# Kernel tuning notes

Measured on AMD Instinct MI355X. Metric: run time of the kernel, lower is better.

The kernel has to match this reference:

```python
import jax, jax.numpy as jnp
import numpy as np

WORD_DICT_SIZE = 50002
POS_DICT_SIZE = 53
DEP_DICT_SIZE = 54
EMB = 128
UNITS = 100
B, T = 256, 256
IN_DIM = 3 * EMB  # 384


def setup_inputs() -> dict:
    key = jax.random.key(0)
    ks = jax.random.split(key, 12)
    words = jax.random.randint(ks[0], (B, T), 1, WORD_DICT_SIZE)
    pos = jax.random.randint(ks[1], (B, T), 1, POS_DICT_SIZE)
    dep = jax.random.randint(ks[2], (B, T), 1, DEP_DICT_SIZE)
    # ragged padding: index 0 is the mask token (mask_zero=True)
    lengths = jax.random.randint(ks[3], (B,), T // 2, T + 1)
    pad = jnp.arange(T)[None, :] >= lengths[:, None]
    words = jnp.where(pad, 0, words)
    pos = jnp.where(pad, 0, pos)
    dep = jnp.where(pad, 0, dep)

    def glorot(k, shape):
        lim = np.sqrt(6.0 / (shape[0] + shape[1]))
        return jax.random.uniform(k, shape, jnp.float32, -lim, lim)

    E_word = glorot(ks[4], (WORD_DICT_SIZE, EMB))
    E_pos = glorot(ks[5], (POS_DICT_SIZE, EMB))
    E_dep = glorot(ks[6], (DEP_DICT_SIZE, EMB))
    W_fwd = glorot(ks[7], (IN_DIM, 4 * UNITS))
    U_fwd = glorot(ks[8], (UNITS, 4 * UNITS))
    W_bwd = glorot(ks[9], (IN_DIM, 4 * UNITS))
    U_bwd = glorot(ks[10], (UNITS, 4 * UNITS))
    # Keras unit_forget_bias=True: forget-gate bias initialized to 1
    b = jnp.zeros((4 * UNITS,), jnp.float32).at[UNITS:2 * UNITS].set(1.0)
    W_out = glorot(ks[11], (2 * UNITS, 1))
    b_out = jnp.zeros((1,), jnp.float32)
    return {"words": words, "pos": pos, "dep": dep,
            "E_word": E_word, "E_pos": E_pos, "E_dep": E_dep,
            "W_fwd": W_fwd, "U_fwd": U_fwd, "b_fwd": b,
            "W_bwd": W_bwd, "U_bwd": U_bwd, "b_bwd": b,
            "W_out": W_out, "b_out": b_out}


def _masked_lstm(x_tbd, mask_tb, W, U, b, reverse):
    """Keras-style masked LSTM. x_tbd: [T,B,D], mask_tb: [T,B].
    Masked steps carry state/output through unchanged (zero_output_for_mask=False)."""
    units = U.shape[0]
    xw = jnp.einsum('tbd,dh->tbh', x_tbd, W) + b  # precompute input projection

    def step(carry, inp):
        h, c = carry
        xw_t, m = inp
        z = xw_t + h @ U
        i, f, g, o = jnp.split(z, 4, axis=-1)
        i = jax.nn.sigmoid(i)
        f = jax.nn.sigmoid(f)
        g = jnp.tanh(g)
        o = jax.nn.sigmoid(o)
        c_new = f * c + i * g
        h_new = o * jnp.tanh(c_new)
        m = m[:, None]
        h2 = jnp.where(m, h_new, h)
        c2 = jnp.where(m, c_new, c)
        return (h2, c2), h2

    h0 = jnp.zeros((x_tbd.shape[1], units), x_tbd.dtype)
    _, hs = jax.lax.scan(step, (h0, h0), (xw, mask_tb), reverse=reverse)
    return hs  # [T,B,units]


def reference(words, pos, dep, E_word, E_pos, E_dep,
              W_fwd, U_fwd, b_fwd, W_bwd, U_bwd, b_bwd, W_out, b_out):
    mask = words != 0  # [B,T]
    x = jnp.concatenate([E_word[words], E_pos[pos], E_dep[dep]], axis=-1)  # [B,T,384]
    xt = jnp.transpose(x, (1, 0, 2))  # [T,B,384]
    mt = mask.T                        # [T,B]
    h_f = _masked_lstm(xt, mt, W_fwd, U_fwd, b_fwd, reverse=False)
    h_b = _masked_lstm(xt, mt, W_bwd, U_bwd, b_bwd, reverse=True)
    h = jnp.concatenate([h_f, h_b], axis=-1)          # [T,B,200]
    h = jnp.transpose(h, (1, 0, 2))                    # [B,T,200]
    out = jax.nn.sigmoid(h @ W_out + b_out)[..., 0]    # [B,T]
    return out
```

## Files before the change

### kernel.cpp

```cpp
#include <hip/hip_runtime.h>
#include <hip/hip_bf16.h>

#define T_LEN 256
#define B_SZ  256
#define EMB   128
#define UNITS 100
#define GATES 400
#define NCOL  800
#define NQ    52

typedef __attribute__((ext_vector_type(8))) short short8v;
typedef __attribute__((ext_vector_type(4))) short short4v;
typedef __attribute__((ext_vector_type(4))) float f32x4;
typedef _Float16 half2v __attribute__((ext_vector_type(2)));

static __device__ __forceinline__ float bf2f(short s) {
    unsigned u = ((unsigned)(unsigned short)s) << 16;
    return __builtin_bit_cast(float, u);
}
static __device__ __forceinline__ short f2bf(float f) {
    return __builtin_bit_cast(short, __float2bfloat16(f));
}
static __device__ __forceinline__ float fast_sigmoid(float x) {
    return 1.f / (1.f + __expf(-x));
}
static __device__ __forceinline__ float fast_tanh(float x) {
    return 1.f - 2.f / (1.f + __expf(2.f * x));
}
static __device__ __forceinline__ float fdot2p(unsigned hp, unsigned up, float c) {
#if __has_builtin(__builtin_amdgcn_fdot2)
    return __builtin_amdgcn_fdot2(__builtin_bit_cast(half2v, hp),
                                  __builtin_bit_cast(half2v, up), c, false);
#else
    const half2v a = __builtin_bit_cast(half2v, hp);
    const half2v b = __builtin_bit_cast(half2v, up);
    return fmaf((float)a[1], (float)b[1], fmaf((float)a[0], (float)b[0], c));
#endif
}

#define PREP_WT_BLOCKS 100
#define PREP_TAB_BLOCKS 107
#define PREP_UPK_BLOCKS 21

__global__ __launch_bounds__(256) void prep(
    const float* __restrict__ Wf, const float* __restrict__ Wb,
    const float* __restrict__ bf_, const float* __restrict__ bb_,
    const float* __restrict__ Ep, const float* __restrict__ Ed,
    const float* __restrict__ Uf, const float* __restrict__ Ub,
    __hip_bfloat16* __restrict__ WbT, float* __restrict__ Ppos,
    float* __restrict__ Pdep, unsigned* __restrict__ Upk, int* __restrict__ flag)
{
    __shared__ short Ap[16 * 32];
    __shared__ short Bp[32 * 16];

    const int bx = blockIdx.x, tid = threadIdx.x;

    if (bx < PREP_WT_BLOCKS) {
        const int base = bx * 1024 + tid * 4;
#pragma unroll
        for (int q = 0; q < 4; ++q) {
            const int id = base + q;
            const int c = id >> 7, k = id & 127;
            const int dir = c >= GATES;
            const int j = c - dir * GATES;
            const float* W = dir ? Wb : Wf;
            WbT[id] = __float2bfloat16(W[k * GATES + j]);
        }
    } else if (bx < PREP_WT_BLOCKS + PREP_TAB_BLOCKS) {
        const int p = bx - PREP_WT_BLOCKS;
        const bool isPos = p < 53;
        const float* Erow = isPos ? (Ep + p * EMB) : (Ed + (size_t)(p - 53) * EMB);
        const int rowoff = isPos ? EMB : 2 * EMB;
        float* dst = isPos ? (Ppos + (size_t)p * NCOL) : (Pdep + (size_t)(p - 53) * NCOL);
        for (int c = tid; c < NCOL; c += 256) {
            const int dir = c >= GATES;
            const int j = c - dir * GATES;
            const float* W = dir ? Wb : Wf;
            float s = 0.f;
            for (int k = 0; k < EMB; ++k)
                s = fmaf(Erow[k], W[(size_t)(rowoff + k) * GATES + j], s);
            if (!isPos) s += (dir ? bb_[j] : bf_[j]);
            dst[c] = s;
        }
    } else if (bx < PREP_WT_BLOCKS + PREP_TAB_BLOCKS + PREP_UPK_BLOCKS) {
        const int p2 = bx - PREP_WT_BLOCKS - PREP_TAB_BLOCKS;
#pragma unroll
        for (int i = 0; i < 8; ++i) {
            const int e = p2 * 2048 + tid * 8 + i;
            if (e < 2 * NQ * GATES) {
                const int dir = e / (NQ * GATES);
                const int rem = e - dir * (NQ * GATES);
                const int q = rem / GATES, col = rem - q * GATES;
                const float* U = dir ? Ub : Uf;
                const int k0 = 2 * q, k1 = 2 * q + 1;
                const float v0 = (k0 < UNITS) ? U[(size_t)k0 * GATES + col] : 0.f;
                const float v1 = (k1 < UNITS) ? U[(size_t)k1 * GATES + col] : 0.f;
                const unsigned lo = (unsigned)(unsigned short)__builtin_bit_cast(short, (_Float16)v0);
                const unsigned hi = (unsigned)(unsigned short)__builtin_bit_cast(short, (_Float16)v1);
                Upk[e] = lo | (hi << 16);
            }
        }
    } else {
        if (tid < 64) {
            for (int e = tid; e < 512; e += 64) {
                const int m = e >> 5, k = e & 31;
                Ap[e] = f2bf((float)((m * 3 + k * 5) % 7 - 3));
            }
            for (int e = tid; e < 512; e += 64) {
                const int k = e >> 4, n = e & 15;
                Bp[e] = f2bf((float)((k * 7 + n * 3) % 5 - 2));
            }
        }
        __syncthreads();
        if (tid < 64) {
            const int l = tid, mn = l & 15, grp = l >> 4;
            float ref[4];
#pragma unroll
            for (int i = 0; i < 4; ++i) {
                const int m = grp * 4 + i;
                float s = 0.f;
                for (int k = 0; k < 32; ++k)
                    s += bf2f(Ap[m * 32 + k]) * bf2f(Bp[k * 16 + mn]);
                ref[i] = s;
            }
            short8v a8, b8;
#pragma unroll
            for (int e = 0; e < 8; ++e) {
                const int k8 = grp * 8 + e;
                a8[e] = Ap[mn * 32 + k8];
                b8[e] = Bp[k8 * 16 + mn];
            }
            f32x4 z = {0.f, 0.f, 0.f, 0.f};
            f32x4 d8 = __builtin_amdgcn_mfma_f32_16x16x32_bf16(a8, b8, z, 0, 0, 0);
            const bool ok8 = (d8[0] == ref[0]) && (d8[1] == ref[1]) &&
                             (d8[2] == ref[2]) && (d8[3] == ref[3]);
            const unsigned long long m8 = __ballot(ok8);
            if (tid == 0) flag[0] = (m8 == ~0ULL) ? 0 : 1;
        }
    }
}

#define MT 64
#define NT 160

__global__ __launch_bounds__(256) void embed_gemm(
    const int* __restrict__ words, const int* __restrict__ pos, const int* __restrict__ dep,
    const float* __restrict__ Ew, const __hip_bfloat16* __restrict__ WbT,
    const float* __restrict__ Ppos, const float* __restrict__ Pdep,
    const int* __restrict__ flag, __hip_bfloat16* __restrict__ xw)
{
    __shared__ __align__(16) short As[MT * 128];
    __shared__ __align__(16) short Bs[NT * 128];
    __shared__ int widx[MT], pidx[MT], didx[MT];

    const int tid = threadIdx.x;
    const int bx = blockIdx.x, by = blockIdx.y;
    const int r0 = bx * MT;
    const int t = r0 >> 8, b0 = r0 & 255;
    const int n0 = by * NT;

    if (tid < MT)             widx[tid]          = words[(size_t)(b0 + tid) * T_LEN + t];
    else if (tid < 2 * MT)    pidx[tid - MT]     = pos[(size_t)(b0 + tid - MT) * T_LEN + t];
    else if (tid < 3 * MT)    didx[tid - 2 * MT] = dep[(size_t)(b0 + tid - 2 * MT) * T_LEN + t];
    __syncthreads();

#pragma unroll
    for (int q = 0; q < 4; ++q) {
        const int ch = tid + q * 256;
        const int row = ch >> 4, c16 = ch & 15;
        const float* src = Ew + (size_t)widx[row] * EMB + c16 * 8;
        const float4 v0 = *reinterpret_cast<const float4*>(src);
        const float4 v1 = *reinterpret_cast<const float4*>(src + 4);
        short8v pk;
        pk[0] = f2bf(v0.x); pk[1] = f2bf(v0.y); pk[2] = f2bf(v0.z); pk[3] = f2bf(v0.w);
        pk[4] = f2bf(v1.x); pk[5] = f2bf(v1.y); pk[6] = f2bf(v1.z); pk[7] = f2bf(v1.w);
        *reinterpret_cast<short8v*>(&As[row * 128 + ((c16 ^ (row & 7)) << 3)]) = pk;
    }
#pragma unroll
    for (int q = 0; q < 10; ++q) {
        const int ch = tid + q * 256;
        const int col = ch >> 4, c16 = ch & 15;
        const short* src = reinterpret_cast<const short*>(WbT) + (size_t)(n0 + col) * 128 + c16 * 8;
        const short8v v = *reinterpret_cast<const short8v*>(src);
        *reinterpret_cast<short8v*>(&Bs[col * 128 + ((c16 ^ (col & 7)) << 3)]) = v;
    }
    __syncthreads();

    const int w = tid >> 6, l = tid & 63;
    const int lr = l & 15, lg = l >> 4;
    const int arow = w * 16 + lr;

    f32x4 acc[10];
#pragma unroll
    for (int ni = 0; ni < 10; ++ni) acc[ni] = f32x4{0.f, 0.f, 0.f, 0.f};

    const int lay = flag[0];

    if (lay == 0) {
#pragma unroll
        for (int kk = 0; kk < 4; ++kk) {
            const int c16 = kk * 4 + lg;
            const short8v a = *reinterpret_cast<const short8v*>(
                &As[arow * 128 + ((c16 ^ (arow & 7)) << 3)]);
#pragma unroll
            for (int ni = 0; ni < 10; ++ni) {
                const int col = ni * 16 + lr;
                const short8v bfr = *reinterpret_cast<const short8v*>(
                    &Bs[col * 128 + ((c16 ^ (col & 7)) << 3)]);
                acc[ni] = __builtin_amdgcn_mfma_f32_16x16x32_bf16(a, bfr, acc[ni], 0, 0, 0);
            }
        }
    } else {
#pragma unroll
        for (int kk = 0; kk < 4; ++kk) {
            const int ch16 = kk * 4 + (lg >> 1);
            const int inner = (lg & 1) * 4;
            const int alo_i = arow * 128 + ((ch16 ^ (arow & 7)) << 3) + inner;
            const int ahi_i = arow * 128 + (((ch16 + 2) ^ (arow & 7)) << 3) + inner;
            const short4v alo = *reinterpret_cast<const short4v*>(&As[alo_i]);
            const short4v ahi = *reinterpret_cast<const short4v*>(&As[ahi_i]);
            short8v a;
            a[0] = alo[0]; a[1] = alo[1]; a[2] = alo[2]; a[3] = alo[3];
            a[4] = ahi[0]; a[5] = ahi[1]; a[6] = ahi[2]; a[7] = ahi[3];
#pragma unroll
            for (int ni = 0; ni < 10; ++ni) {
                const int col = ni * 16 + lr;
                const int blo_i = col * 128 + ((ch16 ^ (col & 7)) << 3) + inner;
                const int bhi_i = col * 128 + (((ch16 + 2) ^ (col & 7)) << 3) + inner;
                const short4v blo = *reinterpret_cast<const short4v*>(&Bs[blo_i]);
                const short4v bhi = *reinterpret_cast<const short4v*>(&Bs[bhi_i]);
                short8v b;
                b[0] = blo[0]; b[1] = blo[1]; b[2] = blo[2]; b[3] = blo[3];
                b[4] = bhi[0]; b[5] = bhi[1]; b[6] = bhi[2]; b[7] = bhi[3];
                acc[ni] = __builtin_amdgcn_mfma_f32_16x16x32_bf16(a, b, acc[ni], 0, 0, 0);
            }
        }
    }

    const int rbase = w * 16 + lg * 4;
    int pix[4], dix[4];
#pragma unroll
    for (int i = 0; i < 4; ++i) { pix[i] = pidx[rbase + i]; dix[i] = didx[rbase + i]; }
#pragma unroll
    for (int ni = 0; ni < 10; ++ni) {
        const int c = n0 + ni * 16 + lr;
#pragma unroll
        for (int i = 0; i < 4; ++i) {
            const float v = acc[ni][i]
                          + Ppos[(size_t)pix[i] * NCOL + c]
                          + Pdep[(size_t)dix[i] * NCOL + c];
            xw[(size_t)(r0 + rbase + i) * NCOL + c] = __float2bfloat16(v);
        }
    }
}

#define BAR() do { \
    asm volatile("s_waitcnt lgkmcnt(0)" ::: "memory"); \
    __builtin_amdgcn_sched_barrier(0); \
    __builtin_amdgcn_s_barrier(); \
    __builtin_amdgcn_sched_barrier(0); \
} while (0)

__global__ __launch_bounds__(512, 1) void lstm_valu(
    const int* __restrict__ words,
    const __hip_bfloat16* __restrict__ xw,
    const unsigned* __restrict__ Upk,
    _Float16* __restrict__ h_f, _Float16* __restrict__ h_b)
{
    const int b = blockIdx.x >> 1, dirv = blockIdx.x & 1;
    _Float16* hout = dirv ? h_b : h_f;
    const int coff = dirv * GATES;
    const unsigned* up = Upk + (size_t)dirv * NQ * GATES;

    __shared__ __align__(16) _Float16 h_sh[104];
    __shared__ float z_sh[GATES];
    __shared__ unsigned char m_sh[T_LEN];

    const int tid = threadIdx.x;
    const bool isCol = tid < GATES;
    const int colid = isCol ? tid : (GATES - 1);

    for (int i = tid; i < T_LEN; i += 512)
        m_sh[i] = (unsigned char)(words[(size_t)b * T_LEN + i] != 0);
    if (tid < 52) reinterpret_cast<unsigned*>(h_sh)[tid] = 0u;

    unsigned upk[NQ];
#pragma unroll
    for (int q = 0; q < NQ; ++q) upk[q] = up[q * GATES + colid];
#pragma unroll
    for (int q = 0; q < NQ; ++q) asm volatile("" : "+v"(upk[q]));

    float c = 0.f, h = 0.f;
    __syncthreads();

    const int t0 = dirv ? (T_LEN - 1) : 0;
    const int dt = dirv ? -1 : 1;
    const short* xs = reinterpret_cast<const short*>(xw);

    short pf = 0;
    if (isCol) pf = xs[((size_t)t0 * B_SZ + b) * NCOL + coff + tid];

    for (int s = 0; s < T_LEN; ++s) {
        const int t = t0 + dt * s;
        int tn = t + dt; tn = tn < 0 ? 0 : (tn > T_LEN - 1 ? T_LEN - 1 : tn);

        short pfn = pf;
        if (isCol) {
            const float zx = bf2f(pf);
            pfn = xs[((size_t)tn * B_SZ + b) * NCOL + coff + tid];
            float a0 = 0.f, a1 = 0.f, a2 = 0.f, a3 = 0.f;
            const uint4* h4 = reinterpret_cast<const uint4*>(h_sh);
#pragma unroll
            for (int qq = 0; qq < 13; ++qq) {
                const uint4 hv = h4[qq];
                a0 = fdot2p(hv.x, upk[4 * qq + 0], a0);
                a1 = fdot2p(hv.y, upk[4 * qq + 1], a1);
                a2 = fdot2p(hv.z, upk[4 * qq + 2], a2);
                a3 = fdot2p(hv.w, upk[4 * qq + 3], a3);
            }
            z_sh[tid] = zx + (a0 + a1) + (a2 + a3);
        }
        pf = pfn;

        BAR();

        if (tid < UNITS) {
            const float zi = z_sh[tid];
            const float zf = z_sh[tid + UNITS];
            const float zg = z_sh[tid + 2 * UNITS];
            const float zo = z_sh[tid + 3 * UNITS];
            const float ig = fast_sigmoid(zi);
            const float fg = fast_sigmoid(zf);
            const float gg = fast_tanh(zg);
            const float og = fast_sigmoid(zo);
            const float cn = fg * c + ig * gg;
            const float hn = og * fast_tanh(cn);
            const bool  m  = m_sh[t] != 0;
            h = m ? hn : h;
            c = m ? cn : c;
            const _Float16 hh = (_Float16)h;
            h_sh[tid] = hh;
            hout[((size_t)t * B_SZ + b) * UNITS + tid] = hh;
        }

        BAR();
    }
}

__global__ __launch_bounds__(256) void out_proj(
    const _Float16* __restrict__ h_f, const _Float16* __restrict__ h_b,
    const float* __restrict__ Wo, const float* __restrict__ bo,
    float* __restrict__ out)
{
    const int tid = threadIdx.x;
    const int g = tid >> 2, sub = tid & 3;
    const int r = blockIdx.x * 64 + g;
    const int t = r >> 8, b = r & 255;

    const _Float16* hf = h_f + (size_t)r * UNITS;
    const _Float16* hb = h_b + (size_t)r * UNITS;

    float s = 0.f;
    const int k0 = sub * 25;
#pragma unroll
    for (int k = 0; k < 25; ++k) s = fmaf((float)hf[k0 + k], Wo[k0 + k], s);
#pragma unroll
    for (int k = 0; k < 25; ++k) s = fmaf((float)hb[k0 + k], Wo[UNITS + k0 + k], s);

    s += __shfl_xor(s, 1);
    s += __shfl_xor(s, 2);

    if (sub == 0)
        out[(size_t)b * T_LEN + t] = 1.f / (1.f + __expf(-(s + bo[0])));
}

extern "C" void kernel_launch(void* const* d_in, const int* in_sizes, int n_in,
                              void* d_out, int out_size, void* d_ws, size_t ws_size,
                              hipStream_t stream)
{
    const int*   words = (const int*)d_in[0];
    const int*   pos   = (const int*)d_in[1];
    const int*   dep   = (const int*)d_in[2];
    const float* Ew    = (const float*)d_in[3];
    const float* Ep    = (const float*)d_in[4];
    const float* Ed    = (const float*)d_in[5];
    const float* Wf    = (const float*)d_in[6];
    const float* Uf    = (const float*)d_in[7];
    const float* bf_   = (const float*)d_in[8];
    const float* Wb    = (const float*)d_in[9];
    const float* Ub    = (const float*)d_in[10];
    const float* bb_   = (const float*)d_in[11];
    const float* Wo    = (const float*)d_in[12];
    const float* bo    = (const float*)d_in[13];
    float* out = (float*)d_out;

    auto alignup = [](size_t x) { return (x + 255) & ~(size_t)255; };
    char* p = (char*)d_ws;
    __hip_bfloat16* xw = (__hip_bfloat16*)p;  p += alignup((size_t)T_LEN * B_SZ * NCOL * 2);
    _Float16* h_f = (_Float16*)p;             p += alignup((size_t)T_LEN * B_SZ * UNITS * 2);
    _Float16* h_b = (_Float16*)p;             p += alignup((size_t)T_LEN * B_SZ * UNITS * 2);
    __hip_bfloat16* WbT = (__hip_bfloat16*)p; p += alignup((size_t)NCOL * 128 * 2);
    float* Ppos = (float*)p;                  p += alignup((size_t)53 * NCOL * 4);
    float* Pdep = (float*)p;                  p += alignup((size_t)54 * NCOL * 4);
    unsigned* Upk = (unsigned*)p;             p += alignup((size_t)2 * NQ * GATES * 4);
    int* flag = (int*)p;

    prep<<<dim3(PREP_WT_BLOCKS + PREP_TAB_BLOCKS + PREP_UPK_BLOCKS + 1), 256, 0, stream>>>(
        Wf, Wb, bf_, bb_, Ep, Ed, Uf, Ub, WbT, Ppos, Pdep, Upk, flag);

    embed_gemm<<<dim3((T_LEN * B_SZ) / MT, NCOL / NT), 256, 0, stream>>>(
        words, pos, dep, Ew, WbT, Ppos, Pdep, flag, xw);

    lstm_valu<<<dim3(B_SZ * 2), 512, 0, stream>>>(words, xw, Upk, h_f, h_b);

    out_proj<<<dim3((T_LEN * B_SZ) / 64), 256, 0, stream>>>(h_f, h_b, Wo, bo, out);
}
```

Before: 350.6 us.

## Interleave gate columns per unit and fuse LSTM cell update via lane shuffles

Permutes the gate columns of U and xw so that the four gates of each unit sit in adjacent lanes. Each lane now computes its own gate activation, with tanh written as 2*sigmoid(2x)-1, and the cell update is done through xor shuffles inside the wavefront. This removes the z_sh shared-memory round trip and one of the two block barriers per timestep, and a double-buffered h replaces the second barrier. Block size drops to 448 threads. The cost is extra index arithmetic in the GEMM epilogue and prep kernel, plus a different tanh formulation.

```diff
diff --git a/kernel.cpp b/kernel.cpp
--- a/kernel.cpp
+++ b/kernel.cpp
@@ -90,11 +90,13 @@
             if (e < 2 * NQ * GATES) {
                 const int dir = e / (NQ * GATES);
                 const int rem = e - dir * (NQ * GATES);
-                const int q = rem / GATES, col = rem - q * GATES;
+                const int q = rem / GATES, jp = rem - q * GATES;
+                const int unit = jp >> 2, gate = jp & 3;
+                const int jorig = gate * UNITS + unit;
                 const float* U = dir ? Ub : Uf;
                 const int k0 = 2 * q, k1 = 2 * q + 1;
-                const float v0 = (k0 < UNITS) ? U[(size_t)k0 * GATES + col] : 0.f;
-                const float v1 = (k1 < UNITS) ? U[(size_t)k1 * GATES + col] : 0.f;
+                const float v0 = (k0 < UNITS) ? U[(size_t)k0 * GATES + jorig] : 0.f;
+                const float v1 = (k1 < UNITS) ? U[(size_t)k1 * GATES + jorig] : 0.f;
                 const unsigned lo = (unsigned)(unsigned short)__builtin_bit_cast(short, (_Float16)v0);
                 const unsigned hi = (unsigned)(unsigned short)__builtin_bit_cast(short, (_Float16)v1);
                 Upk[e] = lo | (hi << 16);
@@ -244,12 +246,16 @@
 #pragma unroll
     for (int ni = 0; ni < 10; ++ni) {
         const int c = n0 + ni * 16 + lr;
+        const int dirg = c >= GATES;
+        const int j = c - dirg * GATES;
+        const int gate = j / UNITS, unit = j - gate * UNITS;
+        const int cperm = dirg * GATES + unit * 4 + gate;
 #pragma unroll
         for (int i = 0; i < 4; ++i) {
             const float v = acc[ni][i]
                           + Ppos[(size_t)pix[i] * NCOL + c]
                           + Pdep[(size_t)dix[i] * NCOL + c];
-            xw[(size_t)(r0 + rbase + i) * NCOL + c] = __float2bfloat16(v);
+            xw[(size_t)(r0 + rbase + i) * NCOL + cperm] = __float2bfloat16(v);
         }
     }
 }
@@ -261,7 +267,7 @@
     __builtin_amdgcn_sched_barrier(0); \
 } while (0)
 
-__global__ __launch_bounds__(512, 1) void lstm_valu(
+__global__ __launch_bounds__(448, 1) void lstm_valu(
     const int* __restrict__ words,
     const __hip_bfloat16* __restrict__ xw,
     const unsigned* __restrict__ Upk,
@@ -272,17 +278,17 @@
     const int coff = dirv * GATES;
     const unsigned* up = Upk + (size_t)dirv * NQ * GATES;
 
-    __shared__ __align__(16) _Float16 h_sh[104];
-    __shared__ float z_sh[GATES];
+    __shared__ __align__(16) _Float16 h_buf[2][104];
     __shared__ unsigned char m_sh[T_LEN];
 
     const int tid = threadIdx.x;
     const bool isCol = tid < GATES;
     const int colid = isCol ? tid : (GATES - 1);
-
-    for (int i = tid; i < T_LEN; i += 512)
+    const int unit = colid >> 2, gate = colid & 3;
+
+    for (int i = tid; i < T_LEN; i += 448)
         m_sh[i] = (unsigned char)(words[(size_t)b * T_LEN + i] != 0);
-    if (tid < 52) reinterpret_cast<unsigned*>(h_sh)[tid] = 0u;
+    if (tid < 104) reinterpret_cast<unsigned*>(&h_buf[0][0])[tid] = 0u;
 
     unsigned upk[NQ];
 #pragma unroll
@@ -298,8 +304,9 @@
     const short* xs = reinterpret_cast<const short*>(xw);
 
     short pf = 0;
-    if (isCol) pf = xs[((size_t)t0 * B_SZ + b) * NCOL + coff + tid];
-
+    if (isCol) pf = xs[((size_t)t0 * B_SZ + b) * NCOL + coff + colid];
+
+    int p = 0;
     for (int s = 0; s < T_LEN; ++s) {
         const int t = t0 + dt * s;
         int tn = t + dt; tn = tn < 0 ? 0 : (tn > T_LEN - 1 ? T_LEN - 1 : tn);
@@ -307,9 +314,9 @@
         short pfn = pf;
         if (isCol) {
             const float zx = bf2f(pf);
-            pfn = xs[((size_t)tn * B_SZ + b) * NCOL + coff + tid];
+            pfn = xs[((size_t)tn * B_SZ + b) * NCOL + coff + colid];
             float a0 = 0.f, a1 = 0.f, a2 = 0.f, a3 = 0.f;
-            const uint4* h4 = reinterpret_cast<const uint4*>(h_sh);
+            const uint4* h4 = reinterpret_cast<const uint4*>(&h_buf[p][0]);
 #pragma unroll
             for (int qq = 0; qq < 13; ++qq) {
                 const uint4 hv = h4[qq];
@@ -318,32 +325,28 @@
                 a2 = fdot2p(hv.z, upk[4 * qq + 2], a2);
                 a3 = fdot2p(hv.w, upk[4 * qq + 3], a3);
             }
-            z_sh[tid] = zx + (a0 + a1) + (a2 + a3);
+            const float z = zx + (a0 + a1) + (a2 + a3);
+            const float zz  = (gate == 2) ? 2.f * z : z;
+            const float sg  = fast_sigmoid(zz);
+            const float act = (gate == 2) ? (2.f * sg - 1.f) : sg;
+            const float v1 = __shfl_xor(act, 1);
+            const float v2 = __shfl_xor(act, 2);
+            const float v3 = __shfl_xor(act, 3);
+            if (gate == 0) {
+                const float cn = v1 * c + act * v2;
+                const float hn = v3 * fast_tanh(cn);
+                const bool m = m_sh[t] != 0;
+                h = m ? hn : h;
+                c = m ? cn : c;
+                const _Float16 hh = (_Float16)h;
+                h_buf[p ^ 1][unit] = hh;
+                hout[((size_t)t * B_SZ + b) * UNITS + unit] = hh;
+            }
         }
         pf = pfn;
 
         BAR();
-
-        if (tid < UNITS) {
-            const float zi = z_sh[tid];
-            const float zf = z_sh[tid + UNITS];
-            const float zg = z_sh[tid + 2 * UNITS];
-            const float zo = z_sh[tid + 3 * UNITS];
-            const float ig = fast_sigmoid(zi);
-            const float fg = fast_sigmoid(zf);
-            const float gg = fast_tanh(zg);
-            const float og = fast_sigmoid(zo);
-            const float cn = fg * c + ig * gg;
-            const float hn = og * fast_tanh(cn);
-            const bool  m  = m_sh[t] != 0;
-            h = m ? hn : h;
-            c = m ? cn : c;
-            const _Float16 hh = (_Float16)h;
-            h_sh[tid] = hh;
-            hout[((size_t)t * B_SZ + b) * UNITS + tid] = hh;
-        }
-
-        BAR();
+        p ^= 1;
     }
 }
 
@@ -411,7 +414,7 @@
     embed_gemm<<<dim3((T_LEN * B_SZ) / MT, NCOL / NT), 256, 0, stream>>>(
         words, pos, dep, Ew, WbT, Ppos, Pdep, flag, xw);
 
-    lstm_valu<<<dim3(B_SZ * 2), 512, 0, stream>>>(words, xw, Upk, h_f, h_b);
+    lstm_valu<<<dim3(B_SZ * 2), 448, 0, stream>>>(words, xw, Upk, h_f, h_b);
 
     out_proj<<<dim3((T_LEN * B_SZ) / 64), 256, 0, stream>>>(h_f, h_b, Wo, bo, out);
 }
```

Result: slower. 403.1 us (+15.0%).
